# Kernel optimization log

Hardware: AMD Instinct MI355X
Metric: run time of the kernel (lower is better)

Reference implementation:

```python
import jax, jax.numpy as jnp
import numpy as np


def setup_inputs() -> dict:
    key = jax.random.key(0)
    k1, k2 = jax.random.split(key)
    B, Q, T, D = 128, 512, 512, 256
    inputs = jax.random.normal(k1, (B, T, D), dtype=jnp.float32)
    query = jax.random.normal(k2, (B, Q, D), dtype=jnp.float32)
    return {"inputs": inputs, "query": query}


def reference(inputs, query):
    # inputs: [B, T, D] (keys == values), query: [B, Q, D]
    D = inputs.shape[2]
    scale = 1.0 / jnp.sqrt(jnp.asarray(D, dtype=inputs.dtype))
    # scores: [B, Q, T]
    scores = jnp.einsum("bqd,btd->bqt", query, inputs) * scale
    weights = jax.nn.softmax(scores, axis=2)
    # attended: [B, Q, D]
    attended = jnp.einsum("bqt,btd->bqd", weights, inputs)
    # pool over query dim -> [B, D]
    return jnp.sum(attended, axis=1)
```

## Files before the change

kernel.cpp:

```cpp
#include <hip/hip_runtime.h>
#include <hip/hip_bf16.h>


typedef __bf16 bf16x8 __attribute__((ext_vector_type(8)));
typedef float  f32x4  __attribute__((ext_vector_type(4)));
typedef unsigned int u32;

#define B_    128
#define Tn    512
#define Dn    256
#define SCALE 0.0625f

#define WAITV4 asm volatile("s_waitcnt vmcnt(4)" ::: "memory")
#define WAITV0 asm volatile("s_waitcnt vmcnt(0)" ::: "memory")
#define BARRAW __builtin_amdgcn_s_barrier()
#define SCHED0 __builtin_amdgcn_sched_barrier(0)

__device__ __forceinline__ int lidx(int row, int ch) {
  return row * 256 + (((ch ^ (row & 31)) & 31) << 3);
}

__device__ __forceinline__ bf16x8 pack8(float4 v0, float4 v1) {
  bf16x8 w;
  w[0] = (__bf16)v0.x; w[1] = (__bf16)v0.y;
  w[2] = (__bf16)v0.z; w[3] = (__bf16)v0.w;
  w[4] = (__bf16)v1.x; w[5] = (__bf16)v1.y;
  w[6] = (__bf16)v1.z; w[7] = (__bf16)v1.w;
  return w;
}

__device__ __forceinline__ void gll16(const __bf16* g, __bf16* l) {
  __builtin_amdgcn_global_load_lds((const u32 __attribute__((address_space(1)))*)g,
                                   (u32 __attribute__((address_space(3)))*)l,
                                   16, 0, 0);
}

__global__ void __launch_bounds__(512) conv_k(const float* __restrict__ inputs,
                                              __bf16* __restrict__ kbf) {
  const int tid = threadIdx.x;
  const int b = blockIdx.x & 127, tile = blockIdx.x >> 7;
#pragma unroll
  for (int i = 0; i < 4; ++i) {
    int c = i * 512 + tid;
    int row = c >> 5, p = c & 31;
    int ch = p ^ (row & 31);
    const float4* s =
        (const float4*)(inputs + ((size_t)b * Tn + tile * 64 + row) * Dn + ch * 8);
    *(bf16x8*)(kbf + (size_t)(b * 8 + tile) * 16384 + (size_t)c * 8) =
        pack8(s[0], s[1]);
  }
}

__global__ void __launch_bounds__(512, 4) attn_fused(
    const __bf16* __restrict__ kbf, const float* __restrict__ query,
    float* __restrict__ out) {
  __shared__ __bf16 smem[4 * 8192 + 1280];
  float* lred = (float*)(smem + 4 * 8192);
  float* cfin = lred + 128;

  const int tid  = threadIdx.x;
  const int b  = blockIdx.x & 127;
  const int qt = blockIdx.x >> 7;

  const int wave = tid >> 6, lane = tid & 63;
  const int quad = lane >> 4, l15 = lane & 15;
  const int qg = wave >> 1;
  const int th = wave & 1;

  const __bf16* ksrc = kbf + (size_t)b * 131072;

  cfin[tid] = 0.f;

#define STAGE(t)                                                        \
  {                                                                     \
    _Pragma("unroll") for (int i_ = 0; i_ < 2; ++i_) {                  \
      int s_ = wave * 2 + i_;                                           \
      gll16(ksrc + (size_t)(t) * 8192 + s_ * 512 + lane * 8,            \
            smem + ((t) & 3) * 8192 + s_ * 512);                        \
    }                                                                   \
  }

  STAGE(0); STAGE(1);

  const float* qsrc = query + ((size_t)b * 512 + qt * 64 + qg * 16 + l15) * Dn;
  bf16x8 a_[8];
#pragma unroll
  for (int dc = 0; dc < 8; ++dc) {
    const float4* p = (const float4*)(qsrc + dc * 32 + quad * 8);
    a_[dc] = pack8(p[0], p[1]);
  }

  STAGE(2); STAGE(3);

  f32x4 acc[16];
  f32x4 zero = {0.f, 0.f, 0.f, 0.f};
#pragma unroll
  for (int i = 0; i < 16; ++i) acc[i] = zero;

#pragma unroll
  for (int p = 0; p < 8; ++p) {
    if (p < 7) { WAITV4; } else { WAITV0; }
    BARRAW;
    SCHED0;
    const __bf16* cur0 = smem + ((2 * p) & 3) * 8192;
    const __bf16* cur1 = smem + ((2 * p + 1) & 3) * 8192;
    __builtin_amdgcn_s_setprio(1);
#pragma unroll
    for (int dc = 0; dc < 8; ++dc) {
      bf16x8 b0 = *(const bf16x8*)(cur0 + lidx(th * 16 + l15, dc * 4 + quad));
      bf16x8 b1 = *(const bf16x8*)(cur1 + lidx(th * 16 + l15, dc * 4 + quad));
      acc[2 * p] = __builtin_amdgcn_mfma_f32_16x16x32_bf16(
          a_[dc], b0, acc[2 * p], 0, 0, 0);
      acc[2 * p + 1] = __builtin_amdgcn_mfma_f32_16x16x32_bf16(
          a_[dc], b1, acc[2 * p + 1], 0, 0, 0);
    }
    __builtin_amdgcn_s_setprio(0);
    SCHED0;
    if (p < 6) { STAGE(2 * p + 4); STAGE(2 * p + 5); }
  }

  float rs[4] = {0.f, 0.f, 0.f, 0.f};
#pragma unroll
  for (int ti = 0; ti < 16; ++ti)
#pragma unroll
    for (int r = 0; r < 4; ++r) {
      float pv = __expf(acc[ti][r] * SCALE);
      acc[ti][r] = pv;
      rs[r] += pv;
    }
#pragma unroll
  for (int off = 1; off <= 8; off <<= 1)
#pragma unroll
    for (int r = 0; r < 4; ++r) rs[r] += __shfl_xor(rs[r], off);

  if (l15 == 0) {
#pragma unroll
    for (int r = 0; r < 4; ++r)
      lred[(qg * 2 + th) * 16 + quad * 4 + r] = rs[r];
  }
  __syncthreads();

  float linv[4];
#pragma unroll
  for (int r = 0; r < 4; ++r) {
    int row = quad * 4 + r;
    linv[r] =
        1.f / (lred[(qg * 2 + 0) * 16 + row] + lred[(qg * 2 + 1) * 16 + row]);
  }

#pragma unroll
  for (int ti = 0; ti < 16; ++ti) {
    float v = 0.f;
#pragma unroll
    for (int r = 0; r < 4; ++r) v += acc[ti][r] * linv[r];
    v += __shfl_xor(v, 16);
    v += __shfl_xor(v, 32);
    if (quad == 0) atomicAdd(&cfin[ti * 32 + th * 16 + l15], v);
  }
  __syncthreads();

  const int dchunk = tid & 31;
  const int tgrp   = tid >> 5;
  float o[8] = {0.f, 0.f, 0.f, 0.f, 0.f, 0.f, 0.f, 0.f};

#pragma unroll 8
  for (int i = 0; i < 32; ++i) {
    int row = tgrp + i * 16;
    int pp = (dchunk ^ (row & 31)) & 31;
    const bf16x8* src = (const bf16x8*)(ksrc + (size_t)(row >> 6) * 16384 +
                                        ((row & 63) * 32 + pp) * 8);
    bf16x8 v = *src;
    float c = cfin[row];
#pragma unroll
    for (int j = 0; j < 8; ++j) o[j] += c * (float)v[j];
  }
  __syncthreads();

  float* ored = (float*)smem;
  f32x4 o0 = {o[0], o[1], o[2], o[3]}, o1 = {o[4], o[5], o[6], o[7]};
  *(f32x4*)&ored[tgrp * 260 + dchunk * 8]     = o0;
  *(f32x4*)&ored[tgrp * 260 + dchunk * 8 + 4] = o1;
  __syncthreads();
  if (tid < 256) {
    float s = 0.f;
#pragma unroll
    for (int g = 0; g < 16; ++g) s += ored[g * 260 + tid];
    atomicAdd(out + (size_t)b * 256 + tid, s);
  }
#undef STAGE
}

__device__ __forceinline__ void kload(const float* __restrict__ src, int tid,
                                      float4* pre) {
#pragma unroll
  for (int i = 0; i < 4; ++i) {
    int u = i * 512 + tid;
    int row = u >> 5, ch = u & 31;
    const float4* p = (const float4*)(src + row * 256 + ch * 8);
    pre[2 * i]     = p[0];
    pre[2 * i + 1] = p[1];
  }
}

__device__ __forceinline__ void kstore(__bf16* dst, int tid,
                                       const float4* pre) {
#pragma unroll
  for (int i = 0; i < 4; ++i) {
    int u = i * 512 + tid;
    int row = u >> 5, ch = u & 31;
    *(bf16x8*)(dst + lidx(row, ch)) = pack8(pre[2 * i], pre[2 * i + 1]);
  }
}

__global__ void __launch_bounds__(512, 2) attn_qk(
    const float* __restrict__ inputs, const float* __restrict__ query,
    float* __restrict__ c_ws) {
  __shared__ __bf16 smem[128 * 256 + 2 * 64 * 256];
  __bf16* Qs = smem;
  __bf16* Kb[2] = {smem + 128 * 256, smem + 128 * 256 + 64 * 256};

  const int tid  = threadIdx.x;
  const int b  = blockIdx.x & 127;
  const int qt = blockIdx.x >> 7;

  const float* qsrc = query  + ((size_t)b * 512 + (size_t)qt * 128) * Dn;
  const float* ksrc = inputs + (size_t)b * Tn * Dn;

  const int wave = tid >> 6, lane = tid & 63;
  const int quad = lane >> 4, l15 = lane & 15;
  const int qg = wave >> 1;
  const int th = wave & 1;

  float4 pre[2][8];
  kload(ksrc, tid, pre[0]);

#pragma unroll
  for (int i = 0; i < 8; ++i) {
    int u = i * 512 + tid;
    int row = u >> 5, ch = u & 31;
    const float4* p = (const float4*)(qsrc + row * 256 + ch * 8);
    *(bf16x8*)(Qs + lidx(row, ch)) = pack8(p[0], p[1]);
  }

  kload(ksrc + (size_t)1 * 64 * Dn, tid, pre[1]);
  __syncthreads();

  kstore(Kb[0], tid, pre[0]);
  kload(ksrc + (size_t)2 * 64 * Dn, tid, pre[0]);
  __syncthreads();

  f32x4 acc[8][2][2];
  f32x4 zero = {0.f, 0.f, 0.f, 0.f};
#pragma unroll
  for (int tt = 0; tt < 8; ++tt)
#pragma unroll
    for (int ct = 0; ct < 2; ++ct) {
      acc[tt][ct][0] = zero;
      acc[tt][ct][1] = zero;
    }

#pragma unroll
  for (int tt = 0; tt < 8; ++tt) {
    if (tt < 7) kstore(Kb[(tt + 1) & 1], tid, pre[(tt + 1) & 1]);
    if (tt < 5) kload(ksrc + (size_t)(tt + 3) * 64 * Dn, tid, pre[(tt + 1) & 1]);

    const __bf16* cur = Kb[tt & 1];
#pragma unroll
    for (int dc = 0; dc < 8; ++dc) {
      bf16x8 a0 = *(const bf16x8*)(Qs + lidx(qg * 32 + l15, dc * 4 + quad));
      bf16x8 a1 = *(const bf16x8*)(Qs + lidx(qg * 32 + 16 + l15, dc * 4 + quad));
#pragma unroll
      for (int ct = 0; ct < 2; ++ct) {
        bf16x8 bb =
            *(const bf16x8*)(cur + lidx(th * 32 + ct * 16 + l15, dc * 4 + quad));
        acc[tt][ct][0] = __builtin_amdgcn_mfma_f32_16x16x32_bf16(
            a0, bb, acc[tt][ct][0], 0, 0, 0);
        acc[tt][ct][1] = __builtin_amdgcn_mfma_f32_16x16x32_bf16(
            a1, bb, acc[tt][ct][1], 0, 0, 0);
      }
    }
    __syncthreads();
  }

  float* lred  = (float*)Kb[0];
  float* cpart = (float*)Kb[0] + 256;

  float rs[2][4];
#pragma unroll
  for (int m = 0; m < 2; ++m)
#pragma unroll
    for (int r = 0; r < 4; ++r) rs[m][r] = 0.f;
#pragma unroll
  for (int tt = 0; tt < 8; ++tt)
#pragma unroll
    for (int ct = 0; ct < 2; ++ct)
#pragma unroll
      for (int m = 0; m < 2; ++m)
#pragma unroll
        for (int r = 0; r < 4; ++r) {
          float p = __expf(acc[tt][ct][m][r] * SCALE);
          acc[tt][ct][m][r] = p;
          rs[m][r] += p;
        }
#pragma unroll
  for (int off = 1; off <= 8; off <<= 1)
#pragma unroll
    for (int m = 0; m < 2; ++m)
#pragma unroll
      for (int r = 0; r < 4; ++r) rs[m][r] += __shfl_xor(rs[m][r], off);

  if (l15 == 0) {
#pragma unroll
    for (int m = 0; m < 2; ++m)
#pragma unroll
      for (int r = 0; r < 4; ++r)
        lred[(qg * 2 + th) * 32 + m * 16 + quad * 4 + r] = rs[m][r];
  }
  __syncthreads();

  float linv[2][4];
#pragma unroll
  for (int m = 0; m < 2; ++m)
#pragma unroll
    for (int r = 0; r < 4; ++r) {
      int row = m * 16 + quad * 4 + r;
      linv[m][r] =
          1.f / (lred[(qg * 2 + 0) * 32 + row] + lred[(qg * 2 + 1) * 32 + row]);
    }

#pragma unroll
  for (int tt = 0; tt < 8; ++tt)
#pragma unroll
    for (int ct = 0; ct < 2; ++ct) {
      float v = 0.f;
#pragma unroll
      for (int m = 0; m < 2; ++m)
#pragma unroll
        for (int r = 0; r < 4; ++r) v += acc[tt][ct][m][r] * linv[m][r];
      v += __shfl_xor(v, 16);
      v += __shfl_xor(v, 32);
      if (quad == 0)
        cpart[qg * 512 + tt * 64 + th * 32 + ct * 16 + l15] = v;
    }
  __syncthreads();

  float* cout = c_ws + ((size_t)qt * B_ + b) * Tn;
#pragma unroll
  for (int t = tid; t < 512; t += 256) {
    if (t < 512)
      cout[t] = cpart[t] + cpart[512 + t] + cpart[1024 + t] + cpart[1536 + t];
  }
}

template <int NSL>
__global__ void __launch_bounds__(256) attn_av(
    const float* __restrict__ inputs, const float* __restrict__ c_ws,
    float* __restrict__ out) {
  __shared__ float cs[64];
  __shared__ float psum[3][256];
  const int bid = blockIdx.x, tid = threadIdx.x;
  const int b = bid & 127, sl = bid >> 7;

  if (tid < 64) {
    int t = sl * 64 + tid;
    float s = 0.f;
#pragma unroll
    for (int i = 0; i < NSL; ++i) s += c_ws[(size_t)(i * B_ + b) * Tn + t];
    cs[tid] = s;
  }
  __syncthreads();

  const int w = tid >> 6, d4 = tid & 63;
  const float4* vb =
      (const float4*)(inputs + ((size_t)b * Tn + sl * 64 + w * 16) * Dn) + d4;
  float ox = 0.f, oy = 0.f, oz = 0.f, ow = 0.f;
#pragma unroll
  for (int j = 0; j < 16; ++j) {
    float c = cs[w * 16 + j];
    float4 v = vb[(size_t)j * 64];
    ox += c * v.x; oy += c * v.y; oz += c * v.z; ow += c * v.w;
  }
  if (w) {
    float4 t = {ox, oy, oz, ow};
    *(float4*)&psum[w - 1][d4 * 4] = t;
  }
  __syncthreads();
  if (!w) {
    float4 p0 = *(float4*)&psum[0][d4 * 4];
    float4 p1 = *(float4*)&psum[1][d4 * 4];
    float4 p2 = *(float4*)&psum[2][d4 * 4];
    float* op = out + b * 256 + d4 * 4;
    atomicAdd(op + 0, ox + p0.x + p1.x + p2.x);
    atomicAdd(op + 1, oy + p0.y + p1.y + p2.y);
    atomicAdd(op + 2, oz + p0.z + p1.z + p2.z);
    atomicAdd(op + 3, ow + p0.w + p1.w + p2.w);
  }
}

extern "C" void kernel_launch(void* const* d_in, const int* in_sizes, int n_in,
                              void* d_out, int out_size, void* d_ws, size_t ws_size,
                              hipStream_t stream) {
  const float* inputs = (const float*)d_in[0];
  const float* query  = (const float*)d_in[1];
  float* out  = (float*)d_out;

  hipMemsetAsync(out, 0, (size_t)B_ * Dn * sizeof(float), stream);

  const size_t kbytes = (size_t)B_ * Tn * Dn * sizeof(__bf16);
  if (ws_size >= kbytes) {
    __bf16* kbf = (__bf16*)d_ws;
    conv_k    <<<dim3(1024), dim3(512), 0, stream>>>(inputs, kbf);
    attn_fused<<<dim3(1024), dim3(512), 0, stream>>>(kbf, query, out);
  } else {
    float* c_ws = (float*)d_ws;
    attn_qk<<<dim3(512), dim3(512), 0, stream>>>(inputs, query, c_ws);
    attn_av<4><<<dim3(1024), dim3(256), 0, stream>>>(inputs, c_ws, out);
  }
}
```

Baseline: 196.4 us.

## Switch QK^T to 32x32x16 MFMA with split-D half staging and double buffering

Rewrites the score GEMM in the fused attention kernel to use 32x32x16 bf16 MFMA tiles, each wave covering 32 query rows against 4 key subtiles. Keys are staged into LDS in D-halves over a two-buffer ping-pong, replacing the four-buffer pipeline that used partial vmcnt waits. Query fragments are reloaded per D-half. The softmax row-sum reduction moves to LDS atomics to fit the new layout. Larger MFMA tiles should cut LDS reads per flop, but the full vmcnt(0) wait plus barrier after every subtile may expose load latency.

```diff
diff --git a/kernel.cpp b/kernel.cpp
--- a/kernel.cpp
+++ b/kernel.cpp
@@ -4,6 +4,7 @@
 
 typedef __bf16 bf16x8 __attribute__((ext_vector_type(8)));
 typedef float  f32x4  __attribute__((ext_vector_type(4)));
+typedef float  f32x16 __attribute__((ext_vector_type(16)));
 typedef unsigned int u32;
 
 #define B_    128
@@ -11,7 +12,6 @@
 #define Dn    256
 #define SCALE 0.0625f
 
-#define WAITV4 asm volatile("s_waitcnt vmcnt(4)" ::: "memory")
 #define WAITV0 asm volatile("s_waitcnt vmcnt(0)" ::: "memory")
 #define BARRAW __builtin_amdgcn_s_barrier()
 #define SCHED0 __builtin_amdgcn_sched_barrier(0)
@@ -54,108 +54,114 @@
 __global__ void __launch_bounds__(512, 4) attn_fused(
     const __bf16* __restrict__ kbf, const float* __restrict__ query,
     float* __restrict__ out) {
-  __shared__ __bf16 smem[4 * 8192 + 1280];
-  float* lred = (float*)(smem + 4 * 8192);
-  float* cfin = lred + 128;
-
-  const int tid  = threadIdx.x;
+  __shared__ __bf16 smem[2 * 16384 + 1152];
+  float* lred = (float*)(smem + 2 * 16384);
+  float* cfin = lred + 64;
+
+  const int tid = threadIdx.x;
   const int b  = blockIdx.x & 127;
   const int qt = blockIdx.x >> 7;
 
   const int wave = tid >> 6, lane = tid & 63;
-  const int quad = lane >> 4, l15 = lane & 15;
-  const int qg = wave >> 1;
-  const int th = wave & 1;
+  const int l31 = lane & 31, hi = lane >> 5;
+  const int qg = wave >> 2;
+  const int tq = wave & 3;
 
   const __bf16* ksrc = kbf + (size_t)b * 131072;
 
   cfin[tid] = 0.f;
-
-#define STAGE(t)                                                        \
-  {                                                                     \
-    _Pragma("unroll") for (int i_ = 0; i_ < 2; ++i_) {                  \
-      int s_ = wave * 2 + i_;                                           \
-      gll16(ksrc + (size_t)(t) * 8192 + s_ * 512 + lane * 8,            \
-            smem + ((t) & 3) * 8192 + s_ * 512);                        \
-    }                                                                   \
-  }
-
-  STAGE(0); STAGE(1);
-
-  const float* qsrc = query + ((size_t)b * 512 + qt * 64 + qg * 16 + l15) * Dn;
-  bf16x8 a_[8];
-#pragma unroll
-  for (int dc = 0; dc < 8; ++dc) {
-    const float4* p = (const float4*)(qsrc + dc * 32 + quad * 8);
-    a_[dc] = pack8(p[0], p[1]);
-  }
-
-  STAGE(2); STAGE(3);
-
-  f32x4 acc[16];
-  f32x4 zero = {0.f, 0.f, 0.f, 0.f};
-#pragma unroll
-  for (int i = 0; i < 16; ++i) acc[i] = zero;
-
-#pragma unroll
-  for (int p = 0; p < 8; ++p) {
-    if (p < 7) { WAITV4; } else { WAITV0; }
+  if (tid < 64) lred[tid] = 0.f;
+
+#define STAGEH(kh, g4, bufoff)                                              \
+  {                                                                         \
+    _Pragma("unroll") for (int i_ = 0; i_ < 4; ++i_) {                      \
+      int u_ = wave * 256 + i_ * 64 + lane;                                 \
+      int tis_ = u_ >> 9, c_ = u_ & 511;                                    \
+      int row_ = c_ >> 4, p_ = c_ & 15;                                     \
+      const __bf16* g_ = ksrc + (size_t)((g4) + tis_) * 8192 + row_ * 256 + \
+                         (p_ + (((kh) ^ (row_ >> 4)) << 4)) * 8;            \
+      gll16(g_, smem + (bufoff) + u_ * 8);                                  \
+    }                                                                       \
+  }
+
+  f32x16 acc[4];
+#pragma unroll
+  for (int s = 0; s < 4; ++s)
+#pragma unroll
+    for (int r = 0; r < 16; ++r) acc[s][r] = 0.f;
+
+  const float* qrow =
+      query + ((size_t)b * 512 + qt * 64 + qg * 32 + l31) * Dn;
+
+#pragma unroll
+  for (int kh = 0; kh < 2; ++kh) {
+    STAGEH(kh, 0, 0);
+
+    bf16x8 a_[8];
+#pragma unroll
+    for (int ks = 0; ks < 8; ++ks) {
+      const float4* p = (const float4*)(qrow + kh * 128 + ks * 16 + hi * 8);
+      a_[ks] = pack8(p[0], p[1]);
+    }
+
+    WAITV0;
     BARRAW;
     SCHED0;
-    const __bf16* cur0 = smem + ((2 * p) & 3) * 8192;
-    const __bf16* cur1 = smem + ((2 * p + 1) & 3) * 8192;
-    __builtin_amdgcn_s_setprio(1);
-#pragma unroll
-    for (int dc = 0; dc < 8; ++dc) {
-      bf16x8 b0 = *(const bf16x8*)(cur0 + lidx(th * 16 + l15, dc * 4 + quad));
-      bf16x8 b1 = *(const bf16x8*)(cur1 + lidx(th * 16 + l15, dc * 4 + quad));
-      acc[2 * p] = __builtin_amdgcn_mfma_f32_16x16x32_bf16(
-          a_[dc], b0, acc[2 * p], 0, 0, 0);
-      acc[2 * p + 1] = __builtin_amdgcn_mfma_f32_16x16x32_bf16(
-          a_[dc], b1, acc[2 * p + 1], 0, 0, 0);
-    }
-    __builtin_amdgcn_s_setprio(0);
-    SCHED0;
-    if (p < 6) { STAGE(2 * p + 4); STAGE(2 * p + 5); }
-  }
-
-  float rs[4] = {0.f, 0.f, 0.f, 0.f};
-#pragma unroll
-  for (int ti = 0; ti < 16; ++ti)
-#pragma unroll
-    for (int r = 0; r < 4; ++r) {
-      float pv = __expf(acc[ti][r] * SCALE);
-      acc[ti][r] = pv;
+
+#pragma unroll
+    for (int s = 0; s < 4; ++s) {
+      if (s < 3) STAGEH(kh, (s + 1) * 4, ((s + 1) & 1) * 16384);
+
+      const __bf16* cur = smem + (s & 1) * 16384 + tq * 4096 + l31 * 128;
+      __builtin_amdgcn_s_setprio(1);
+#pragma unroll
+      for (int ks = 0; ks < 8; ++ks) {
+        bf16x8 bb =
+            *(const bf16x8*)(cur + ((((ks * 2 + hi) ^ (l31 & 15)) & 15) << 3));
+        acc[s] = __builtin_amdgcn_mfma_f32_32x32x16_bf16(a_[ks], bb, acc[s],
+                                                         0, 0, 0);
+      }
+      __builtin_amdgcn_s_setprio(0);
+      WAITV0;
+      BARRAW;
+      SCHED0;
+    }
+  }
+
+  float rs[16];
+#pragma unroll
+  for (int r = 0; r < 16; ++r) rs[r] = 0.f;
+#pragma unroll
+  for (int s = 0; s < 4; ++s)
+#pragma unroll
+    for (int r = 0; r < 16; ++r) {
+      float pv = __expf(acc[s][r] * SCALE);
+      acc[s][r] = pv;
       rs[r] += pv;
     }
 #pragma unroll
-  for (int off = 1; off <= 8; off <<= 1)
-#pragma unroll
-    for (int r = 0; r < 4; ++r) rs[r] += __shfl_xor(rs[r], off);
-
-  if (l15 == 0) {
-#pragma unroll
-    for (int r = 0; r < 4; ++r)
-      lred[(qg * 2 + th) * 16 + quad * 4 + r] = rs[r];
-  }
-  __syncthreads();
-
-  float linv[4];
-#pragma unroll
-  for (int r = 0; r < 4; ++r) {
-    int row = quad * 4 + r;
-    linv[r] =
-        1.f / (lred[(qg * 2 + 0) * 16 + row] + lred[(qg * 2 + 1) * 16 + row]);
-  }
-
-#pragma unroll
-  for (int ti = 0; ti < 16; ++ti) {
+  for (int off = 1; off <= 16; off <<= 1)
+#pragma unroll
+    for (int r = 0; r < 16; ++r) rs[r] += __shfl_xor(rs[r], off);
+
+  if (l31 == 0) {
+#pragma unroll
+    for (int r = 0; r < 16; ++r)
+      atomicAdd(&lred[qg * 32 + (r & 3) + 8 * (r >> 2) + 4 * hi], rs[r]);
+  }
+  __syncthreads();
+
+  float linv[16];
+#pragma unroll
+  for (int r = 0; r < 16; ++r)
+    linv[r] = 1.f / lred[qg * 32 + (r & 3) + 8 * (r >> 2) + 4 * hi];
+
+#pragma unroll
+  for (int s = 0; s < 4; ++s) {
     float v = 0.f;
 #pragma unroll
-    for (int r = 0; r < 4; ++r) v += acc[ti][r] * linv[r];
-    v += __shfl_xor(v, 16);
-    v += __shfl_xor(v, 32);
-    if (quad == 0) atomicAdd(&cfin[ti * 32 + th * 16 + l15], v);
+    for (int r = 0; r < 16; ++r) v += acc[s][r] * linv[r];
+    atomicAdd(&cfin[(s * 4 + tq) * 32 + l31], v);
   }
   __syncthreads();
 
@@ -187,7 +193,7 @@
     for (int g = 0; g < 16; ++g) s += ored[g * 260 + tid];
     atomicAdd(out + (size_t)b * 256 + tid, s);
   }
-#undef STAGE
+#undef STAGEH
 }
 
 __device__ __forceinline__ void kload(const float* __restrict__ src, int tid,
```

Result: slower. 225.0 us (+14.6%).
